# Kernel tuning notes

Measured on AMD Instinct MI355X. Metric: run time of the kernel, lower is better.

The kernel has to match this reference:

```python
import jax, jax.numpy as jnp
import numpy as np

B, S, E = 2, 1024, 1024
H, DH = 16, 64           # num_heads, key_dim = E // H
MAXLEN = 2048            # config.max_sequence_length -> table size 2*MAXLEN-1


def setup_inputs() -> dict:
    key = jax.random.key(0)
    ks = jax.random.split(key, 13)
    sc = 1.0 / np.sqrt(E)
    return {
        "query": jax.random.normal(ks[0], (B, S, E), jnp.float32),
        "key": jax.random.normal(ks[1], (B, S, E), jnp.float32),
        "value": jax.random.normal(ks[2], (B, S, E), jnp.float32),
        "Wq": jax.random.normal(ks[3], (E, E), jnp.float32) * sc,
        "bq": jnp.zeros((E,), jnp.float32),
        "Wk": jax.random.normal(ks[4], (E, E), jnp.float32) * sc,
        "bk": jnp.zeros((E,), jnp.float32),
        "Wv": jax.random.normal(ks[5], (E, E), jnp.float32) * sc,
        "bv": jnp.zeros((E,), jnp.float32),
        "Wo": jax.random.normal(ks[6], (E, E), jnp.float32) * sc,
        "bo": jnp.zeros((E,), jnp.float32),
        "rel_pos_emb": jax.random.normal(ks[7], (2 * MAXLEN - 1, DH), jnp.float32) * 0.02,
        "rel_pos_bias": jnp.zeros((2 * MAXLEN - 1,), jnp.float32),
    }


def _split_heads(x):
    # [B, S, E] -> [B, H, S, DH]
    return x.reshape(B, S, H, DH).transpose(0, 2, 1, 3)


def _relative_shift(x):
    # x: [B, H, S, S]; pad one zero column on the left of the last dim,
    # reshape to [B, H, S+1, S], drop the first row -> [B, H, S, S]
    x = jnp.pad(x, ((0, 0), (0, 0), (0, 0), (1, 0)))
    x = x.reshape(B, H, S + 1, S)
    return x[:, :, 1:, :]


def reference(query, key, value, Wq, bq, Wk, bk, Wv, bv, Wo, bo,
              rel_pos_emb, rel_pos_bias):
    q = _split_heads(query @ Wq + bq) / jnp.sqrt(jnp.float32(DH))  # [B,H,S,DH]
    k = _split_heads(key @ Wk + bk)                                 # [B,H,S,DH]
    v = _split_heads(value @ Wv + bv)                               # [B,H,S,DH]

    scores = jnp.einsum("bhid,bhjd->bhij", q, k)  # [B,H,S,S]

    # relative position term (gather + skew, as in the original call())
    pos_ids = jnp.arange(S)[:, None] - jnp.arange(S)[None, :] + (MAXLEN - 1)  # [S,S]
    rpe = rel_pos_emb[pos_ids]    # [S, S, DH]
    rpb = rel_pos_bias[pos_ids]   # [S, S]
    rel = jnp.einsum("bhid,ijd->bhij", q, rpe)  # [B,H,S,S]
    rel = _relative_shift(rel)
    scores = scores + rel + rpb   # rpb broadcasts over [B,H]

    weights = jax.nn.softmax(scores, axis=-1)
    out = jnp.einsum("bhij,bhjd->bhid", weights, v)  # [B,H,S,DH]
    out = out.transpose(0, 2, 1, 3).reshape(B, S, E)
    return out @ Wo + bo
```

## Files before the change

### kernel.cpp

```cpp
#include <hip/hip_runtime.h>

typedef unsigned short u16;
typedef __bf16 bf16_t;
typedef bf16_t bf16x8 __attribute__((ext_vector_type(8)));
typedef u16 u16x8 __attribute__((ext_vector_type(8)));
typedef float f32x4 __attribute__((ext_vector_type(4)));

#define DEVI __device__ __forceinline__


DEVI u16 f2bf(float f) {
    unsigned u = __builtin_bit_cast(unsigned, f);
    u = (u + 0x7FFFu + ((u >> 16) & 1u)) >> 16;
    return (u16)u;
}
DEVI float bf2f(u16 b) {
    unsigned u = ((unsigned)b) << 16;
    return __builtin_bit_cast(float, u);
}
DEVI f32x4 mfma16(u16x8 a, u16x8 b, f32x4 c) {
    return __builtin_amdgcn_mfma_f32_16x16x32_bf16(
        __builtin_bit_cast(bf16x8, a), __builtin_bit_cast(bf16x8, b), c, 0, 0, 0);
}
DEVI void gl2lds(const u16* g, u16* l) {
    __builtin_amdgcn_global_load_lds(
        (__attribute__((address_space(1))) void*)g,
        (__attribute__((address_space(3))) void*)l, 16, 0, 0);
}

__global__ __launch_bounds__(256) void cvt_kernel(
    const float* __restrict__ q, const float* __restrict__ k, const float* __restrict__ v,
    const float* __restrict__ emb, const float* __restrict__ rpb,
    u16* __restrict__ xq, u16* __restrict__ xk, u16* __restrict__ xv, u16* __restrict__ embb,
    u16* __restrict__ Brel2)
{
    const long NQ = 2097152;
    const long NE = 262080;
    if (blockIdx.x >= 6400) {
        int u = (blockIdx.x - 6400) * 256 + threadIdx.x;
        int i = u & 1023;
        if (i <= 1022)
            Brel2[((long)u << 10) + i + 1] = f2bf(rpb[2046]);
        return;
    }
    long i4 = ((long)blockIdx.x * 256 + threadIdx.x) * 4;
    if (i4 < 3 * NQ) {
        int which = (int)(i4 >> 21);
        long off = i4 & (NQ - 1);
        const float* src = which == 0 ? q : (which == 1 ? k : v);
        u16* dst = which == 0 ? xq : (which == 1 ? xk : xv);
        float4 f = *(const float4*)(src + off);
        ushort4 o; o.x = f2bf(f.x); o.y = f2bf(f.y); o.z = f2bf(f.z); o.w = f2bf(f.w);
        *(ushort4*)(dst + off) = o;
    } else {
        long off = i4 - 3 * NQ;
        if (off < NE) {
            float4 f = *(const float4*)(emb + off);
            ushort4 o; o.x = f2bf(f.x); o.y = f2bf(f.y); o.z = f2bf(f.z); o.w = f2bf(f.w);
            *(ushort4*)(embb + off) = o;
        }
    }
}

__global__ __launch_bounds__(256) void wt_kernel(
    const float* __restrict__ w0, const float* __restrict__ w1,
    const float* __restrict__ w2, const float* __restrict__ w3,
    u16* __restrict__ t0, u16* __restrict__ t1, u16* __restrict__ t2, u16* __restrict__ t3)
{
    int z = blockIdx.z;
    const float* W = z == 0 ? w0 : (z == 1 ? w1 : (z == 2 ? w2 : w3));
    u16* T = z == 0 ? t0 : (z == 1 ? t1 : (z == 2 ? t2 : t3));
    __shared__ float tile[64][65];
    int k0 = blockIdx.y * 64, n0 = blockIdx.x * 64;
    int tx = threadIdx.x, ty = threadIdx.y;
    for (int r = ty; r < 64; r += 4)
        tile[r][tx] = W[(long)(k0 + r) * 1024 + n0 + tx];
    __syncthreads();
    for (int r = ty; r < 64; r += 4)
        T[(long)(n0 + r) * 1024 + k0 + tx] = f2bf(tile[tx][r]);
}

template<int MT>
__global__ __launch_bounds__(256) void gemm_kernel(
    const u16* __restrict__ A0, const u16* __restrict__ A1, const u16* __restrict__ A2,
    const u16* __restrict__ W0, const u16* __restrict__ W1, const u16* __restrict__ W2,
    const float* __restrict__ bias0, const float* __restrict__ bias1, const float* __restrict__ bias2,
    u16* __restrict__ o0, u16* __restrict__ o1, u16* __restrict__ o2,
    float* __restrict__ ofp, int mode_base)
{
    int z = blockIdx.z;
    int mode = mode_base + z;
    const u16* A = z == 0 ? A0 : (z == 1 ? A1 : A2);
    const u16* W = z == 0 ? W0 : (z == 1 ? W1 : W2);
    const float* bias = z == 0 ? bias0 : (z == 1 ? bias1 : bias2);
    u16* ob = z == 0 ? o0 : (z == 1 ? o1 : o2);

    constexpr int MROWS = MT * 32;
    __shared__ u16 la[MROWS * 32];
    __shared__ u16 lw[128 * 32];

    int m0 = blockIdx.y * MROWS, n0 = blockIdx.x * 128;
    int t = threadIdx.x, lane = t & 63, wid = t >> 6;
    int l15 = lane & 15, quad = lane >> 4;
    int wm = (wid >> 1) * (MT * 16), wn = (wid & 1) * 64;
    int sr = lane >> 2, sp = lane & 3;

    f32x4 acc[MT][4] = {};

    for (int k0 = 0; k0 < 1024; k0 += 32) {
        __syncthreads();
#pragma unroll
        for (int q = 0; q < MT / 2; q++) {
            int r = wid * (MT * 8) + q * 16 + sr;
            int c = sp ^ ((r >> 1) & 3);
            gl2lds(A + (long)(m0 + r) * 1024 + k0 + c * 8, la + (wid * (MT * 8) + q * 16) * 32);
        }
#pragma unroll
        for (int q = 0; q < 2; q++) {
            int r = wid * 32 + q * 16 + sr;
            int c = sp ^ ((r >> 1) & 3);
            gl2lds(W + (long)(n0 + r) * 1024 + k0 + c * 8, lw + (wid * 32 + q * 16) * 32);
        }
        __syncthreads();
        u16x8 af[MT], bfr[4];
#pragma unroll
        for (int mt = 0; mt < MT; mt++) {
            int r = wm + mt * 16 + l15;
            af[mt] = *(const u16x8*)&la[r * 32 + ((quad ^ ((r >> 1) & 3)) * 8)];
        }
#pragma unroll
        for (int nt = 0; nt < 4; nt++) {
            int r = wn + nt * 16 + l15;
            bfr[nt] = *(const u16x8*)&lw[r * 32 + ((quad ^ ((r >> 1) & 3)) * 8)];
        }
#pragma unroll
        for (int mt = 0; mt < MT; mt++)
#pragma unroll
            for (int nt = 0; nt < 4; nt++)
                acc[mt][nt] = mfma16(af[mt], bfr[nt], acc[mt][nt]);
    }

#pragma unroll
    for (int mt = 0; mt < MT; mt++)
#pragma unroll
        for (int nt = 0; nt < 4; nt++)
#pragma unroll
            for (int reg = 0; reg < 4; reg++) {
                int gm = m0 + wm + mt * 16 + quad * 4 + reg;
                int gn = n0 + wn + nt * 16 + l15;
                float val = acc[mt][nt][reg] + bias[gn];
                if (mode == 0) {
                    val *= 0.125f;
                    long o = ((long)((gm >> 10) * 16 + (gn >> 6)) << 16) + ((gm & 1023) << 6) + (gn & 63);
                    ob[o] = f2bf(val);
                } else if (mode == 1) {
                    long o = ((long)((gm >> 10) * 16 + (gn >> 6)) << 16) + ((gm & 1023) << 6) + (gn & 63);
                    ob[o] = f2bf(val);
                } else if (mode == 2) {
                    long o = ((long)((gm >> 10) * 16 + (gn >> 6)) << 16) + ((long)(gn & 63) << 10) + (gm & 1023);
                    ob[o] = f2bf(val);
                } else {
                    ofp[(long)gm * 1024 + gn] = val;
                }
            }
}

__global__ __launch_bounds__(256) void gc_kernel(
    const u16* __restrict__ qb, const u16* __restrict__ embb,
    const float* __restrict__ rpb, u16* __restrict__ Brel2)
{
    int u0 = blockIdx.x * 16;
    int i0 = u0 & 1023;
    int t = threadIdx.x, lane = t & 63, wid = t >> 6;
    int l15 = lane & 15, quad = lane >> 4;

    u16x8 aq[2];
    long qoff = (long)(u0 + l15) * 64 + quad * 8;
    aq[0] = *(const u16x8*)&qb[qoff];
    aq[1] = *(const u16x8*)&qb[qoff + 32];

    for (int tt = wid; tt < 65; tt += 4) {
        int w0 = tt * 16;
        long ebase = (long)(1024 + i0 + w0 + l15) * 64 + quad * 8;
        u16x8 b0 = *(const u16x8*)&embb[ebase];
        u16x8 b1 = *(const u16x8*)&embb[ebase + 32];
        f32x4 c = {};
        c = mfma16(aq[0], b0, c);
        c = mfma16(aq[1], b1, c);
#pragma unroll
        for (int reg = 0; reg < 4; reg++) {
            int r = quad * 4 + reg;
            int cc = w0 + l15 - r;
            if (cc < 0 || cc > 1023) continue;
            int u = u0 + r;
            int i = u & 1023;
            if (cc <= i) {
                Brel2[((long)u << 10) + (i - cc)] = f2bf(c[reg] + rpb[cc + 2047]);
            } else if (i >= 1) {
                Brel2[((long)(u - 1) << 10) + (i + 1024 - cc)] = f2bf(c[reg] + rpb[cc + 1022]);
            }
        }
    }
}

__global__ __launch_bounds__(256, 4) void flash_kernel(
    const u16* __restrict__ qb, const u16* __restrict__ kb, const u16* __restrict__ vT,
    const u16* __restrict__ Brel2,
    float* __restrict__ Po, float* __restrict__ Pm, float* __restrict__ Pl)
{
    int itile = blockIdx.x;
    int bh = blockIdx.y;
    int js = blockIdx.z;
    int t = threadIdx.x, lane = t & 63, wid = t >> 6;
    int l15 = lane & 15, quad = lane >> 4;
    int i0w = itile * 64 + wid * 16;

    __shared__ u16 lds_k[64 * 64];
    __shared__ u16 lds_v[64 * 64];
    __shared__ u16 lds_p[4][16][72];

    int sr8 = lane >> 3, sp8 = lane & 7;

    u16x8 aq[2];
    {
        long qoff = ((long)(bh * 1024) + i0w + l15) * 64 + quad * 8;
        aq[0] = *(const u16x8*)&qb[qoff];
        aq[1] = *(const u16x8*)&qb[qoff + 32];
    }
    float m_r[4], l_r[4];
    f32x4 o_acc[4] = {};
#pragma unroll
    for (int r = 0; r < 4; r++) { m_r[r] = -1e30f; l_r[r] = 0.f; }

    const u16* kbase = kb + (long)bh * 65536;
    const u16* vbase = vT + (long)bh * 65536;
    const u16* bbase = Brel2 + ((long)bh << 20);

    for (int jt = 0; jt < 8; jt++) {
        int j0 = js * 512 + jt * 64;
        __syncthreads();
#pragma unroll
        for (int q = 0; q < 2; q++) {
            int r = wid * 16 + q * 8 + sr8;
            int c = sp8 ^ (r & 7);
            gl2lds(kbase + (long)(j0 + r) * 64 + c * 8, lds_k + (wid * 16 + q * 8) * 64);
            gl2lds(vbase + (long)r * 1024 + j0 + c * 8, lds_v + (wid * 16 + q * 8) * 64);
        }
        __syncthreads();

        f32x4 s_acc[4];
#pragma unroll
        for (int nt = 0; nt < 4; nt++) {
            int r = nt * 16 + l15;
            u16x8 b0 = *(const u16x8*)&lds_k[r * 64 + ((quad ^ (r & 7)) * 8)];
            u16x8 b1 = *(const u16x8*)&lds_k[r * 64 + (((quad + 4) ^ (r & 7)) * 8)];
            f32x4 c = {};
            c = mfma16(aq[0], b0, c);
            c = mfma16(aq[1], b1, c);
            s_acc[nt] = c;
        }

#pragma unroll
        for (int nt = 0; nt < 4; nt++) {
            int jj = j0 + nt * 16 + l15;
#pragma unroll
            for (int reg = 0; reg < 4; reg++) {
                int ii = i0w + quad * 4 + reg;
                s_acc[nt][reg] += bf2f(bbase[((long)ii << 10) + jj]);
            }
        }

#pragma unroll
        for (int reg = 0; reg < 4; reg++) {
            float mx = fmaxf(fmaxf(s_acc[0][reg], s_acc[1][reg]), fmaxf(s_acc[2][reg], s_acc[3][reg]));
            for (int off = 1; off < 16; off <<= 1) mx = fmaxf(mx, __shfl_xor(mx, off, 64));
            float mnew = fmaxf(m_r[reg], mx);
            float alpha = __expf(m_r[reg] - mnew);
            float rs = 0.f;
#pragma unroll
            for (int nt = 0; nt < 4; nt++) {
                float p = __expf(s_acc[nt][reg] - mnew);
                s_acc[nt][reg] = p;
                rs += p;
            }
            for (int off = 1; off < 16; off <<= 1) rs += __shfl_xor(rs, off, 64);
            l_r[reg] = l_r[reg] * alpha + rs;
            m_r[reg] = mnew;
#pragma unroll
            for (int dt = 0; dt < 4; dt++) o_acc[dt][reg] *= alpha;
        }

#pragma unroll
        for (int nt = 0; nt < 4; nt++)
#pragma unroll
            for (int reg = 0; reg < 4; reg++)
                lds_p[wid][quad * 4 + reg][nt * 16 + l15] = f2bf(s_acc[nt][reg]);

        u16x8 pf0 = *(const u16x8*)&lds_p[wid][l15][quad * 8];
        u16x8 pf1 = *(const u16x8*)&lds_p[wid][l15][quad * 8 + 32];
#pragma unroll
        for (int dt = 0; dt < 4; dt++) {
            int r = dt * 16 + l15;
            u16x8 v0 = *(const u16x8*)&lds_v[r * 64 + ((quad ^ (r & 7)) * 8)];
            u16x8 v1 = *(const u16x8*)&lds_v[r * 64 + (((quad + 4) ^ (r & 7)) * 8)];
            o_acc[dt] = mfma16(pf0, v0, o_acc[dt]);
            o_acc[dt] = mfma16(pf1, v1, o_acc[dt]);
        }
    }

    int blk = (js * 32 + bh) * 16 + itile;
    float* PoB = Po + (long)blk * 4096;
#pragma unroll
    for (int dt = 0; dt < 4; dt++)
#pragma unroll
        for (int reg = 0; reg < 4; reg++) {
            int rr = wid * 16 + quad * 4 + reg;
            PoB[rr * 64 + dt * 16 + l15] = o_acc[dt][reg];
        }
    if (l15 == 0) {
#pragma unroll
        for (int reg = 0; reg < 4; reg++) {
            int rr = wid * 16 + quad * 4 + reg;
            Pm[blk * 64 + rr] = m_r[reg];
            Pl[blk * 64 + rr] = l_r[reg];
        }
    }
}

__global__ __launch_bounds__(256) void combine_kernel(
    const float* __restrict__ Po, const float* __restrict__ Pm, const float* __restrict__ Pl,
    u16* __restrict__ attn)
{
    int itile = blockIdx.x, bh = blockIdx.y;
    int t = threadIdx.x;
    int c = t & 63, rg = t >> 6;
    int blk0 = bh * 16 + itile;
    int blk1 = (32 + bh) * 16 + itile;
    int b = bh >> 4, h = bh & 15;
    for (int rr = rg; rr < 64; rr += 4) {
        float m0 = Pm[blk0 * 64 + rr], m1 = Pm[blk1 * 64 + rr];
        float ms = fmaxf(m0, m1);
        float e0 = __expf(m0 - ms), e1 = __expf(m1 - ms);
        float l = Pl[blk0 * 64 + rr] * e0 + Pl[blk1 * 64 + rr] * e1;
        float o = Po[(long)blk0 * 4096 + rr * 64 + c] * e0
                + Po[(long)blk1 * 4096 + rr * 64 + c] * e1;
        int ii = itile * 64 + rr;
        attn[((long)(b * 1024 + ii)) * 1024 + h * 64 + c] = f2bf(o / l);
    }
}

extern "C" void kernel_launch(void* const* d_in, const int* in_sizes, int n_in,
                              void* d_out, int out_size, void* d_ws, size_t ws_size,
                              hipStream_t stream)
{
    const float* query = (const float*)d_in[0];
    const float* key_  = (const float*)d_in[1];
    const float* value = (const float*)d_in[2];
    const float* Wq = (const float*)d_in[3];
    const float* bq = (const float*)d_in[4];
    const float* Wk = (const float*)d_in[5];
    const float* bk = (const float*)d_in[6];
    const float* Wv = (const float*)d_in[7];
    const float* bv = (const float*)d_in[8];
    const float* Wo = (const float*)d_in[9];
    const float* bo = (const float*)d_in[10];
    const float* emb = (const float*)d_in[11];
    const float* rpb = (const float*)d_in[12];

    char* ws = (char*)d_ws;
    u16* xq   = (u16*)(ws + 0);
    u16* xk   = (u16*)(ws + 4194304);
    u16* xv   = (u16*)(ws + 8388608);
    u16* WqT  = (u16*)(ws + 12582912);
    u16* WkT  = (u16*)(ws + 14680064);
    u16* WvT  = (u16*)(ws + 16777216);
    u16* embb = (u16*)(ws + 18874368);
    u16* WoT  = (u16*)(ws + 19922944);
    u16* qb   = (u16*)(ws + 22020096);
    u16* kb   = (u16*)(ws + 26214400);
    u16* vT   = (u16*)(ws + 30408704);
    u16* Brel2= (u16*)(ws + 34603008);
    float* Po = (float*)(ws + 0);
    float* Pm = (float*)(ws + 16777216);
    float* Pl = (float*)(ws + 17039360);
    u16* attn = (u16*)(ws + 22020096);

    cvt_kernel<<<6528, 256, 0, stream>>>(query, key_, value, emb, rpb, xq, xk, xv, embb, Brel2);
    wt_kernel<<<dim3(16, 16, 4), dim3(64, 4), 0, stream>>>(Wq, Wk, Wv, Wo, WqT, WkT, WvT, WoT);
    gemm_kernel<4><<<dim3(8, 16, 3), 256, 0, stream>>>(xq, xk, xv, WqT, WkT, WvT,
                                                       bq, bk, bv, qb, kb, vT, nullptr, 0);
    gc_kernel<<<2048, 256, 0, stream>>>(qb, embb, rpb, Brel2);
    flash_kernel<<<dim3(16, 32, 2), 256, 0, stream>>>(qb, kb, vT, Brel2, Po, Pm, Pl);
    combine_kernel<<<dim3(16, 32), 256, 0, stream>>>(Po, Pm, Pl, attn);
    gemm_kernel<2><<<dim3(8, 32, 1), 256, 0, stream>>>(attn, nullptr, nullptr, WoT, nullptr, nullptr,
                                                       bo, nullptr, nullptr,
                                                       nullptr, nullptr, nullptr, (float*)d_out, 3);
}
```

Baseline: 251.8 us.

## Store relative bias unskewed via LDS staging and apply skew in flash reads

After: 264.3 us. 1.05x slower.

```diff
diff --git a/kernel.cpp b/kernel.cpp
--- a/kernel.cpp
+++ b/kernel.cpp
@@ -30,19 +30,11 @@
 
 __global__ __launch_bounds__(256) void cvt_kernel(
     const float* __restrict__ q, const float* __restrict__ k, const float* __restrict__ v,
-    const float* __restrict__ emb, const float* __restrict__ rpb,
-    u16* __restrict__ xq, u16* __restrict__ xk, u16* __restrict__ xv, u16* __restrict__ embb,
-    u16* __restrict__ Brel2)
+    const float* __restrict__ emb,
+    u16* __restrict__ xq, u16* __restrict__ xk, u16* __restrict__ xv, u16* __restrict__ embb)
 {
     const long NQ = 2097152;
     const long NE = 262080;
-    if (blockIdx.x >= 6400) {
-        int u = (blockIdx.x - 6400) * 256 + threadIdx.x;
-        int i = u & 1023;
-        if (i <= 1022)
-            Brel2[((long)u << 10) + i + 1] = f2bf(rpb[2046]);
-        return;
-    }
     long i4 = ((long)blockIdx.x * 256 + threadIdx.x) * 4;
     if (i4 < 3 * NQ) {
         int which = (int)(i4 >> 21);
@@ -167,12 +159,14 @@
 
 __global__ __launch_bounds__(256) void gc_kernel(
     const u16* __restrict__ qb, const u16* __restrict__ embb,
-    const float* __restrict__ rpb, u16* __restrict__ Brel2)
+    const float* __restrict__ rpb, u16* __restrict__ Bskew)
 {
     int u0 = blockIdx.x * 16;
     int i0 = u0 & 1023;
     int t = threadIdx.x, lane = t & 63, wid = t >> 6;
     int l15 = lane & 15, quad = lane >> 4;
+
+    __shared__ u16 lds_s[16][1032];
 
     u16x8 aq[2];
     long qoff = (long)(u0 + l15) * 64 + quad * 8;
@@ -191,21 +185,26 @@
         for (int reg = 0; reg < 4; reg++) {
             int r = quad * 4 + reg;
             int cc = w0 + l15 - r;
-            if (cc < 0 || cc > 1023) continue;
-            int u = u0 + r;
-            int i = u & 1023;
-            if (cc <= i) {
-                Brel2[((long)u << 10) + (i - cc)] = f2bf(c[reg] + rpb[cc + 2047]);
-            } else if (i >= 1) {
-                Brel2[((long)(u - 1) << 10) + (i + 1024 - cc)] = f2bf(c[reg] + rpb[cc + 1022]);
+            if ((unsigned)cc <= 1023u) {
+                int i = i0 + r;
+                float rb = rpb[cc + (cc <= i ? 2047 : 1022)];
+                lds_s[r][cc] = f2bf(c[reg] + rb);
             }
         }
+    }
+    __syncthreads();
+#pragma unroll
+    for (int rd = 0; rd < 8; rd++) {
+        int r = rd * 2 + (t >> 7);
+        int ch = t & 127;
+        u16x8 vv = *(const u16x8*)&lds_s[r][ch * 8];
+        *(u16x8*)&Bskew[((long)(u0 + r) << 10) + ch * 8] = vv;
     }
 }
 
 __global__ __launch_bounds__(256, 4) void flash_kernel(
     const u16* __restrict__ qb, const u16* __restrict__ kb, const u16* __restrict__ vT,
-    const u16* __restrict__ Brel2,
+    const u16* __restrict__ Bskew, const float* __restrict__ rpb,
     float* __restrict__ Po, float* __restrict__ Pm, float* __restrict__ Pl)
 {
     int itile = blockIdx.x;
@@ -221,6 +220,8 @@
 
     int sr8 = lane >> 3, sp8 = lane & 7;
 
+    float rpb2046 = rpb[2046];
+
     u16x8 aq[2];
     {
         long qoff = ((long)(bh * 1024) + i0w + l15) * 64 + quad * 8;
@@ -234,7 +235,7 @@
 
     const u16* kbase = kb + (long)bh * 65536;
     const u16* vbase = vT + (long)bh * 65536;
-    const u16* bbase = Brel2 + ((long)bh << 20);
+    const u16* bbase = Bskew + ((long)bh << 20);
 
     for (int jt = 0; jt < 8; jt++) {
         int j0 = js * 512 + jt * 64;
@@ -262,11 +263,30 @@
 
 #pragma unroll
         for (int nt = 0; nt < 4; nt++) {
-            int jj = j0 + nt * 16 + l15;
-#pragma unroll
-            for (int reg = 0; reg < 4; reg++) {
-                int ii = i0w + quad * 4 + reg;
-                s_acc[nt][reg] += bf2f(bbase[((long)ii << 10) + jj]);
+            int jn0 = j0 + nt * 16;
+            int jj = jn0 + l15;
+            if (jn0 + 15 <= i0w) {
+#pragma unroll
+                for (int reg = 0; reg < 4; reg++) {
+                    int ii = i0w + quad * 4 + reg;
+                    s_acc[nt][reg] += bf2f(bbase[((long)ii << 10) + (ii - jj)]);
+                }
+            } else if (jn0 >= i0w + 17) {
+#pragma unroll
+                for (int reg = 0; reg < 4; reg++) {
+                    int ii = i0w + quad * 4 + reg;
+                    s_acc[nt][reg] += bf2f(bbase[((long)(ii + 1) << 10) + (ii + 1025 - jj)]);
+                }
+            } else {
+#pragma unroll
+                for (int reg = 0; reg < 4; reg++) {
+                    int ii = i0w + quad * 4 + reg;
+                    float a;
+                    if (jj <= ii)          a = bf2f(bbase[((long)ii << 10) + (ii - jj)]);
+                    else if (jj == ii + 1) a = rpb2046;
+                    else                   a = bf2f(bbase[((long)(ii + 1) << 10) + (ii + 1025 - jj)]);
+                    s_acc[nt][reg] += a;
+                }
             }
         }
 
@@ -379,18 +399,18 @@
     u16* qb   = (u16*)(ws + 22020096);
     u16* kb   = (u16*)(ws + 26214400);
     u16* vT   = (u16*)(ws + 30408704);
-    u16* Brel2= (u16*)(ws + 34603008);
+    u16* Bskew= (u16*)(ws + 34603008);
     float* Po = (float*)(ws + 0);
     float* Pm = (float*)(ws + 16777216);
     float* Pl = (float*)(ws + 17039360);
     u16* attn = (u16*)(ws + 22020096);
 
-    cvt_kernel<<<6528, 256, 0, stream>>>(query, key_, value, emb, rpb, xq, xk, xv, embb, Brel2);
+    cvt_kernel<<<6400, 256, 0, stream>>>(query, key_, value, emb, xq, xk, xv, embb);
     wt_kernel<<<dim3(16, 16, 4), dim3(64, 4), 0, stream>>>(Wq, Wk, Wv, Wo, WqT, WkT, WvT, WoT);
     gemm_kernel<4><<<dim3(8, 16, 3), 256, 0, stream>>>(xq, xk, xv, WqT, WkT, WvT,
                                                        bq, bk, bv, qb, kb, vT, nullptr, 0);
-    gc_kernel<<<2048, 256, 0, stream>>>(qb, embb, rpb, Brel2);
-    flash_kernel<<<dim3(16, 32, 2), 256, 0, stream>>>(qb, kb, vT, Brel2, Po, Pm, Pl);
+    gc_kernel<<<2048, 256, 0, stream>>>(qb, embb, rpb, Bskew);
+    flash_kernel<<<dim3(16, 32, 2), 256, 0, stream>>>(qb, kb, vT, Bskew, rpb, Po, Pm, Pl);
     combine_kernel<<<dim3(16, 32), 256, 0, stream>>>(Po, Pm, Pl, attn);
     gemm_kernel<2><<<dim3(8, 32, 1), 256, 0, stream>>>(attn, nullptr, nullptr, WoT, nullptr, nullptr,
                                                        bo, nullptr, nullptr,
```
